# Kernel tuning notes

Hardware: AMD Instinct MI355X
Metric: run time of the kernel (lower is better)

The kernel has to match this reference:

```python
import jax, jax.numpy as jnp
import numpy as np

# Module hyperparameters (from init_kwargs / HGSELLayer defaults)
D_MODEL = 512
D_FF = 2048
N_EXPERTS = 64
K_ACTIVE = 2
N_HASHES = 4
LAYER_ID = 0
SALT = 0.0
BUCKET_SCALE = 8.0        # hash bucket width for projection-based hashing
CAPACITY_FACTOR = 1.25    # per-expert capacity slack (hash routing is near-uniform)


def setup_inputs() -> dict:
    key = jax.random.key(0)
    k0, k1, k2, k3 = jax.random.split(key, 4)
    B, S = 4, 2048
    hidden_states = jax.random.normal(k0, (B, S, D_MODEL), dtype=jnp.float32)
    # Fixed (non-learned) hash projection vectors of the MultiHashRouter
    W_hash = jax.random.normal(k1, (N_HASHES, D_MODEL), dtype=jnp.float32) / np.float32(np.sqrt(D_MODEL))
    # Expert bank parameters: per-expert MLP d_model -> d_ff -> d_model
    W1 = jax.random.normal(k2, (N_EXPERTS, D_MODEL, D_FF), dtype=jnp.float32) * np.float32(1.0 / np.sqrt(D_MODEL))
    b1 = jnp.zeros((N_EXPERTS, D_FF), dtype=jnp.float32)
    W2 = jax.random.normal(k3, (N_EXPERTS, D_FF, D_MODEL), dtype=jnp.float32) * np.float32(1.0 / np.sqrt(D_FF))
    b2 = jnp.zeros((N_EXPERTS, D_MODEL), dtype=jnp.float32)
    return {"hidden_states": hidden_states, "W_hash": W_hash, "W1": W1, "b1": b1, "W2": W2, "b2": b2}


def reference(hidden_states, W_hash, W1, b1, W2, b2):
    B, S, D = hidden_states.shape
    T = B * S
    x = hidden_states.reshape(T, D)

    # ---- MultiHashRouter: hash-based top-k expert selection (non-learned routing) ----
    scores = x @ W_hash.T                                   # [T, n_hashes]
    buckets = jnp.mod(
        jnp.floor(scores * BUCKET_SCALE + SALT).astype(jnp.int32) + LAYER_ID,
        N_EXPERTS,
    )                                                       # [T, n_hashes]
    selected = buckets[:, :K_ACTIVE]                        # [T, k]
    flat_e = selected.reshape(-1)                           # [T*k]

    # ---- Dispatch: capacity-bucketed gather into per-expert buffers ----
    C = int(np.ceil(T * K_ACTIVE / N_EXPERTS * CAPACITY_FACTOR))
    oh = jax.nn.one_hot(flat_e, N_EXPERTS, dtype=jnp.int32)          # [T*k, E]
    pos = jnp.sum((jnp.cumsum(oh, axis=0) - 1) * oh, axis=1)         # slot within expert
    valid = pos < C                                                   # [T*k]
    pos_c = jnp.clip(pos, 0, C - 1)
    x_rep = jnp.repeat(x, K_ACTIVE, axis=0)                           # [T*k, D]
    buf = jnp.zeros((N_EXPERTS, C, D), dtype=x.dtype).at[flat_e, pos_c].add(
        jnp.where(valid[:, None], x_rep, 0.0)
    )                                                                 # [E, C, D]

    # ---- ExpertBank: grouped per-expert MLP (gelu) ----
    h = jax.nn.gelu(jnp.einsum('ecd,edf->ecf', buf, W1) + b1[:, None, :], approximate=False)
    y = jnp.einsum('ecf,efd->ecd', h, W2) + b2[:, None, :]            # [E, C, D]

    # ---- Combine: gather back per token-expert pair, uniform mean over k ----
    out_pairs = jnp.where(valid[:, None], y[flat_e, pos_c], 0.0)      # [T*k, D]
    out = out_pairs.reshape(T, K_ACTIVE, D).mean(axis=1)              # [T, D]
    return out.reshape(B, S, D)
```

## Files before the change

### kernel.cpp

```cpp
#include <hip/hip_runtime.h>
#include <hip/hip_bf16.h>

#define T_TOK 8192
#define NSLOT 16384
#define DM 512
#define DF 2048
#define NEXP 64
#define CAP 320
#define MP 384

typedef __bf16 bf16_t;
typedef __bf16 bf16x8 __attribute__((ext_vector_type(8)));
typedef float floatx4 __attribute__((ext_vector_type(4)));

__global__ __launch_bounds__(256) void k_scores(const float* __restrict__ x,
        const float* __restrict__ Wh, int* __restrict__ e_arr, int* __restrict__ inv)
{
    int tid = threadIdx.x;
    if (tid < 10) inv[blockIdx.x * 10 + tid] = -1;
    int wid = tid >> 6, lane = tid & 63;
    int t = blockIdx.x * 4 + wid;
    const float4* xp = (const float4*)(x + (size_t)t * DM);
    float4 x0 = xp[lane * 2], x1 = xp[lane * 2 + 1];
    const float4* w0p = (const float4*)(Wh);
    const float4* w1p = (const float4*)(Wh + DM);
    float4 a0 = w0p[lane * 2], a1 = w0p[lane * 2 + 1];
    float4 b0 = w1p[lane * 2], b1 = w1p[lane * 2 + 1];
    float s0 = x0.x*a0.x + x0.y*a0.y + x0.z*a0.z + x0.w*a0.w
             + x1.x*a1.x + x1.y*a1.y + x1.z*a1.z + x1.w*a1.w;
    float s1 = x0.x*b0.x + x0.y*b0.y + x0.z*b0.z + x0.w*b0.w
             + x1.x*b1.x + x1.y*b1.y + x1.z*b1.z + x1.w*b1.w;
    #pragma unroll
    for (int off = 32; off; off >>= 1) {
        s0 += __shfl_xor(s0, off);
        s1 += __shfl_xor(s1, off);
    }
    if (lane == 0) {
        int q0 = ((int)floorf(s0 * 8.0f)) & 63;
        int q1 = ((int)floorf(s1 * 8.0f)) & 63;
        e_arr[2 * t]     = q0;
        e_arr[2 * t + 1] = q1;
    }
}

__global__ __launch_bounds__(256) void k_hist(const int* __restrict__ e_arr,
        int* __restrict__ rank_arr, int* __restrict__ hist_g)
{
    __shared__ int se[256];
    __shared__ int hist[64];
    int tid = threadIdx.x;
    if (tid < 64) hist[tid] = 0;
    __syncthreads();
    int s = blockIdx.x * 256 + tid;
    int e = e_arr[s];
    se[tid] = e;
    atomicAdd(&hist[e], 1);
    __syncthreads();
    int cnt = 0;
    for (int j = 0; j < 255; ++j)
        if (j < tid && se[j] == e) cnt++;
    rank_arr[s] = cnt;
    if (tid < 64) hist_g[blockIdx.x * 64 + tid] = hist[tid];
}

__global__ __launch_bounds__(256) void k_pos(const int* __restrict__ e_arr,
        const int* __restrict__ rank_arr, const int* __restrict__ hist_g,
        int* __restrict__ pos_arr, int* __restrict__ inv)
{
    __shared__ int base[64];
    int tid = threadIdx.x, c = blockIdx.x;
    if (tid < 64) {
        int run = 0;
        for (int cc = 0; cc < c; ++cc) run += hist_g[cc * 64 + tid];
        base[tid] = run;
    }
    __syncthreads();
    int s = c * 256 + tid;
    int e = e_arr[s];
    int p = base[e] + rank_arr[s];
    pos_arr[s] = p;
    if (p < CAP) inv[e * CAP + p] = s;
}

__global__ __launch_bounds__(256) void k_buf(const float* __restrict__ x,
        const int* __restrict__ inv, bf16_t* __restrict__ buf)
{
    int tid = threadIdx.x;
    int r = blockIdx.x * 4 + (tid >> 6);
    int lane = tid & 63;
    int e = r / MP, row = r % MP;
    int s = (row < CAP) ? inv[e * CAP + row] : -1;
    union { uint4 u; bf16_t h[8]; } pk;
    if (s >= 0) {
        int t = s >> 1;
        const float* xr = x + (size_t)t * DM + lane * 8;
        float4 f0 = *(const float4*)xr;
        float4 f1 = *(const float4*)(xr + 4);
        pk.h[0] = (bf16_t)f0.x; pk.h[1] = (bf16_t)f0.y;
        pk.h[2] = (bf16_t)f0.z; pk.h[3] = (bf16_t)f0.w;
        pk.h[4] = (bf16_t)f1.x; pk.h[5] = (bf16_t)f1.y;
        pk.h[6] = (bf16_t)f1.z; pk.h[7] = (bf16_t)f1.w;
    } else {
        pk.u.x = 0; pk.u.y = 0; pk.u.z = 0; pk.u.w = 0;
    }
    *(uint4*)(buf + (size_t)r * DM + lane * 8) = pk.u;
}

template<int M_TOT, int OSTR, int N_DIM, int K_DIM, bool GELU, bool OUT_BF16>
__global__ __launch_bounds__(256) void gemm_fused(const bf16_t* __restrict__ A,
        const float* __restrict__ B, const float* __restrict__ bias,
        void* __restrict__ OutP)
{
    constexpr int MT = (M_TOT + 127) / 128;
    constexpr int NT = N_DIM / 128;
    int bx = blockIdx.x;
    int e  = bx / (MT * NT);
    int rem = bx % (MT * NT);
    int mt = rem / NT;
    int nt = rem % NT;

    const bf16_t* Ae = A + (size_t)e * MP * K_DIM + (size_t)mt * 128 * K_DIM;
    const float*  Be = B + (size_t)e * K_DIM * N_DIM + nt * 128;
    const float*  be = bias + (size_t)e * N_DIM + nt * 128;

    __shared__ __align__(16) bf16_t As[128 * 64];
    __shared__ __align__(16) bf16_t Bs[128 * 64];

    int tid = threadIdx.x;
    int lane = tid & 63;
    int wid = tid >> 6;
    int qm = lane & 15;
    int quad = lane >> 4;
    int wm = (wid >> 1) * 64;
    int wn = (wid & 1) * 64;

    int srow = lane >> 3;
    int gl = (lane & 7) ^ srow;
    const bf16_t* aPtr = Ae + (size_t)(wid * 32 + srow) * K_DIM + gl * 8;

    int bkg = tid & 7;
    int bn  = (tid >> 3) * 4;
    const float* bPtr = Be + (size_t)(bkg * 8) * N_DIM + bn;

    uint4  aR[4];
    float4 bR[8];
    #pragma unroll
    for (int c = 0; c < 4; ++c)
        aR[c] = *(const uint4*)(aPtr + (size_t)c * 8 * K_DIM);
    #pragma unroll
    for (int p = 0; p < 8; ++p)
        bR[p] = *(const float4*)(bPtr + (size_t)p * N_DIM);

    floatx4 acc[4][4];
    #pragma unroll
    for (int i = 0; i < 4; ++i)
        #pragma unroll
        for (int j = 0; j < 4; ++j) acc[i][j] = (floatx4)0.0f;

    #pragma unroll 2
    for (int kk = 0; kk < K_DIM; kk += 64) {
        __syncthreads();
        #pragma unroll
        for (int c = 0; c < 4; ++c)
            *(uint4*)(As + ((wid * 4 + c) * 64 + lane) * 8) = aR[c];
        #pragma unroll
        for (int i = 0; i < 4; ++i) {
            union { uint4 u; bf16_t h[8]; } pk;
            #pragma unroll
            for (int p = 0; p < 8; ++p)
                pk.h[p] = (bf16_t)(((const float*)&bR[p])[i]);
            int r = bn + i;
            *(uint4*)(Bs + ((r * 8 + (bkg ^ (r & 7))) * 8)) = pk.u;
        }
        if (kk + 64 < K_DIM) {
            #pragma unroll
            for (int c = 0; c < 4; ++c)
                aR[c] = *(const uint4*)(aPtr + (size_t)c * 8 * K_DIM + (kk + 64));
            #pragma unroll
            for (int p = 0; p < 8; ++p)
                bR[p] = *(const float4*)(bPtr + (size_t)(kk + 64 + p) * N_DIM);
        }
        __syncthreads();
        #pragma unroll
        for (int ks = 0; ks < 2; ++ks) {
            bf16x8 af[4], bfr[4];
            #pragma unroll
            for (int i = 0; i < 4; ++i) {
                int r = wm + i * 16 + qm;
                int pg = r * 8 + ((ks * 4 + quad) ^ (r & 7));
                af[i] = *(const bf16x8*)(As + pg * 8);
            }
            #pragma unroll
            for (int j = 0; j < 4; ++j) {
                int r = wn + j * 16 + qm;
                int pg = r * 8 + ((ks * 4 + quad) ^ (r & 7));
                bfr[j] = *(const bf16x8*)(Bs + pg * 8);
            }
            #pragma unroll
            for (int i = 0; i < 4; ++i)
                #pragma unroll
                for (int j = 0; j < 4; ++j)
                    acc[i][j] = __builtin_amdgcn_mfma_f32_16x16x32_bf16(
                        bfr[j], af[i], acc[i][j], 0, 0, 0);
        }
    }

    #pragma unroll
    for (int i = 0; i < 4; ++i) {
        int gm = mt * 128 + wm + i * 16 + qm;
        if (gm < M_TOT) {
            #pragma unroll
            for (int j = 0; j < 4; ++j) {
                int ln0 = wn + j * 16 + quad * 4;
                float4 bz = *(const float4*)(be + ln0);
                float v[4];
                #pragma unroll
                for (int r = 0; r < 4; ++r) {
                    float t = acc[i][j][r] + ((const float*)&bz)[r];
                    if (GELU) t = 0.5f * t * (1.0f + erff(t * 0.70710678118654752f));
                    v[r] = t;
                }
                size_t idx = ((size_t)e * OSTR + gm) * N_DIM + nt * 128 + ln0;
                if (OUT_BF16) {
                    union { uint2 u; bf16_t h[4]; } pk;
                    pk.h[0] = (bf16_t)v[0]; pk.h[1] = (bf16_t)v[1];
                    pk.h[2] = (bf16_t)v[2]; pk.h[3] = (bf16_t)v[3];
                    *(uint2*)((bf16_t*)OutP + idx) = pk.u;
                } else {
                    float4 o; o.x = v[0]; o.y = v[1]; o.z = v[2]; o.w = v[3];
                    *(float4*)((float*)OutP + idx) = o;
                }
            }
        }
    }
}

__global__ __launch_bounds__(256) void k_gather(const float* __restrict__ y,
        const int* __restrict__ e_arr, const int* __restrict__ pos_arr,
        float* __restrict__ out)
{
    int tid = threadIdx.x;
    int t = blockIdx.x * 4 + (tid >> 6);
    int lane = tid & 63;
    float a[8];
    #pragma unroll
    for (int i = 0; i < 8; ++i) a[i] = 0.0f;
    #pragma unroll
    for (int k = 0; k < 2; ++k) {
        int s = 2 * t + k;
        int e = e_arr[s], p = pos_arr[s];
        if (p < CAP) {
            const float* yr = y + ((size_t)e * CAP + p) * DM + lane * 8;
            float4 f0 = *(const float4*)yr;
            float4 f1 = *(const float4*)(yr + 4);
            a[0] += f0.x; a[1] += f0.y; a[2] += f0.z; a[3] += f0.w;
            a[4] += f1.x; a[5] += f1.y; a[6] += f1.z; a[7] += f1.w;
        }
    }
    float4 o0, o1;
    o0.x = a[0] * 0.5f; o0.y = a[1] * 0.5f; o0.z = a[2] * 0.5f; o0.w = a[3] * 0.5f;
    o1.x = a[4] * 0.5f; o1.y = a[5] * 0.5f; o1.z = a[6] * 0.5f; o1.w = a[7] * 0.5f;
    float* orow = out + (size_t)t * DM + lane * 8;
    *(float4*)orow = o0;
    *(float4*)(orow + 4) = o1;
}

extern "C" void kernel_launch(void* const* d_in, const int* in_sizes, int n_in,
                              void* d_out, int out_size, void* d_ws, size_t ws_size,
                              hipStream_t stream)
{
    const float* x  = (const float*)d_in[0];
    const float* Wh = (const float*)d_in[1];
    const float* W1 = (const float*)d_in[2];
    const float* b1 = (const float*)d_in[3];
    const float* W2 = (const float*)d_in[4];
    const float* b2 = (const float*)d_in[5];
    float* out = (float*)d_out;

    char* p = (char*)d_ws;
    int*    e_arr  = (int*)p;    p += (size_t)NSLOT * 4;
    int*    rank_a = (int*)p;    p += (size_t)NSLOT * 4;
    int*    hist_g = (int*)p;    p += (size_t)64 * 64 * 4;
    int*    pos_a  = (int*)p;    p += (size_t)NSLOT * 4;
    int*    inv    = (int*)p;    p += (size_t)NEXP * CAP * 4;
    bf16_t* buf    = (bf16_t*)p;
    float*  ybuf   = (float*)p;  p += (size_t)NEXP * CAP * DM * 4;
    bf16_t* hbuf   = (bf16_t*)p; p += (size_t)NEXP * MP * DF * 2;

    k_scores<<<2048, 256, 0, stream>>>(x, Wh, e_arr, inv);
    k_hist<<<64, 256, 0, stream>>>(e_arr, rank_a, hist_g);
    k_pos<<<64, 256, 0, stream>>>(e_arr, rank_a, hist_g, pos_a, inv);
    k_buf<<<NEXP * MP / 4, 256, 0, stream>>>(x, inv, buf);

    gemm_fused<CAP, MP, DF, DM, true, true>
        <<<NEXP * 3 * (DF / 128), 256, 0, stream>>>(buf, W1, b1, (void*)hbuf);

    gemm_fused<CAP, CAP, DM, DF, false, false>
        <<<NEXP * 3 * (DM / 128), 256, 0, stream>>>(hbuf, W2, b2, (void*)ybuf);

    k_gather<<<2048, 256, 0, stream>>>(ybuf, e_arr, pos_a, out);
}
```

Measured before the change: 902.7 us.

## Double-buffer LDS in expert GEMMs, reorder grid, emit bf16 expert outputs

Rewrites the grouped expert GEMM with double-buffered shared memory and two register stages, so global loads run three tiles ahead and only one barrier is needed per K-tile. The block index now iterates experts in the inner dimension and M tiles in the outer one, which changes scheduling and weight reuse across blocks. The second GEMM writes bf16 instead of fp32 and leaves the b2 bias to the gather kernel, cutting the output write and gather read traffic in half. This adds LDS use and register pressure (launch bounds 256,2) and lowers the precision of the expert outputs.

```diff
diff --git a/kernel.cpp b/kernel.cpp
--- a/kernel.cpp
+++ b/kernel.cpp
@@ -12,6 +12,12 @@
 typedef __bf16 bf16_t;
 typedef __bf16 bf16x8 __attribute__((ext_vector_type(8)));
 typedef float floatx4 __attribute__((ext_vector_type(4)));
+
+__device__ __forceinline__ void lgkm0_barrier() {
+    asm volatile("s_waitcnt lgkmcnt(0)" ::: "memory");
+    __builtin_amdgcn_s_barrier();
+    asm volatile("" ::: "memory");
+}
 
 __global__ __launch_bounds__(256) void k_scores(const float* __restrict__ x,
         const float* __restrict__ Wh, int* __restrict__ e_arr, int* __restrict__ inv)
@@ -106,25 +112,24 @@
     *(uint4*)(buf + (size_t)r * DM + lane * 8) = pk.u;
 }
 
-template<int M_TOT, int OSTR, int N_DIM, int K_DIM, bool GELU, bool OUT_BF16>
-__global__ __launch_bounds__(256) void gemm_fused(const bf16_t* __restrict__ A,
+template<int M_TOT, int OSTR, int N_DIM, int K_DIM, bool GELU, bool BIAS, bool OUT_BF16>
+__global__ __launch_bounds__(256, 2) void gemm_pipe(const bf16_t* __restrict__ A,
         const float* __restrict__ B, const float* __restrict__ bias,
         void* __restrict__ OutP)
 {
-    constexpr int MT = (M_TOT + 127) / 128;
     constexpr int NT = N_DIM / 128;
+    constexpr int NTILE = K_DIM / 64;
     int bx = blockIdx.x;
-    int e  = bx / (MT * NT);
-    int rem = bx % (MT * NT);
-    int mt = rem / NT;
-    int nt = rem % NT;
+    int mt = bx / (NEXP * NT);
+    int g  = bx % (NEXP * NT);
+    int e  = g / NT;
+    int nt = g % NT;
 
     const bf16_t* Ae = A + (size_t)e * MP * K_DIM + (size_t)mt * 128 * K_DIM;
     const float*  Be = B + (size_t)e * K_DIM * N_DIM + nt * 128;
-    const float*  be = bias + (size_t)e * N_DIM + nt * 128;
-
-    __shared__ __align__(16) bf16_t As[128 * 64];
-    __shared__ __align__(16) bf16_t Bs[128 * 64];
+
+    __shared__ __align__(16) bf16_t As[2][128 * 64];
+    __shared__ __align__(16) bf16_t Bs[2][128 * 64];
 
     int tid = threadIdx.x;
     int lane = tid & 63;
@@ -137,19 +142,32 @@
     int srow = lane >> 3;
     int gl = (lane & 7) ^ srow;
     const bf16_t* aPtr = Ae + (size_t)(wid * 32 + srow) * K_DIM + gl * 8;
-
     int bkg = tid & 7;
     int bn  = (tid >> 3) * 4;
     const float* bPtr = Be + (size_t)(bkg * 8) * N_DIM + bn;
 
-    uint4  aR[4];
-    float4 bR[8];
-    #pragma unroll
-    for (int c = 0; c < 4; ++c)
-        aR[c] = *(const uint4*)(aPtr + (size_t)c * 8 * K_DIM);
-    #pragma unroll
-    for (int p = 0; p < 8; ++p)
-        bR[p] = *(const float4*)(bPtr + (size_t)p * N_DIM);
+    uint4  aS[2][4];
+    float4 bS[2][8];
+
+    #define LOAD_A(st, t_) { _Pragma("unroll") \
+        for (int c = 0; c < 4; ++c) \
+            aS[st][c] = *(const uint4*)(aPtr + (size_t)c * 8 * K_DIM + (t_) * 64); }
+    #define LOAD_B(st, t_) { _Pragma("unroll") \
+        for (int p = 0; p < 8; ++p) \
+            bS[st][p] = *(const float4*)(bPtr + (size_t)((t_) * 64 + p) * N_DIM); }
+    #define STAGE(lb, st) { \
+        _Pragma("unroll") \
+        for (int c = 0; c < 4; ++c) \
+            *(uint4*)(&As[lb][((wid * 4 + c) * 64 + lane) * 8]) = aS[st][c]; \
+        _Pragma("unroll") \
+        for (int i = 0; i < 4; ++i) { \
+            union { uint4 u; bf16_t h[8]; } pk; \
+            _Pragma("unroll") \
+            for (int p = 0; p < 8; ++p) \
+                pk.h[p] = (bf16_t)(((const float*)&bS[st][p])[i]); \
+            int r_ = bn + i; \
+            *(uint4*)(&Bs[lb][(r_ * 8 + (bkg ^ (r_ & 7))) * 8]) = pk.u; \
+        } }
 
     floatx4 acc[4][4];
     #pragma unroll
@@ -157,30 +175,19 @@
         #pragma unroll
         for (int j = 0; j < 4; ++j) acc[i][j] = (floatx4)0.0f;
 
-    #pragma unroll 2
-    for (int kk = 0; kk < K_DIM; kk += 64) {
-        __syncthreads();
-        #pragma unroll
-        for (int c = 0; c < 4; ++c)
-            *(uint4*)(As + ((wid * 4 + c) * 64 + lane) * 8) = aR[c];
-        #pragma unroll
-        for (int i = 0; i < 4; ++i) {
-            union { uint4 u; bf16_t h[8]; } pk;
-            #pragma unroll
-            for (int p = 0; p < 8; ++p)
-                pk.h[p] = (bf16_t)(((const float*)&bR[p])[i]);
-            int r = bn + i;
-            *(uint4*)(Bs + ((r * 8 + (bkg ^ (r & 7))) * 8)) = pk.u;
+    LOAD_A(0, 0); LOAD_B(0, 0);
+    STAGE(0, 0);
+    if (NTILE > 1) { LOAD_A(1, 1); LOAD_B(1, 1); }
+    if (NTILE > 2) { LOAD_A(0, 2); LOAD_B(0, 2); }
+    lgkm0_barrier();
+
+    for (int t = 0; t < NTILE; ++t) {
+        int cur = t & 1;
+        if (t + 1 < NTILE) {
+            int s = (t + 1) & 1;
+            STAGE(cur ^ 1, s);
+            if (t + 3 < NTILE) { LOAD_A(s, t + 3); LOAD_B(s, t + 3); }
         }
-        if (kk + 64 < K_DIM) {
-            #pragma unroll
-            for (int c = 0; c < 4; ++c)
-                aR[c] = *(const uint4*)(aPtr + (size_t)c * 8 * K_DIM + (kk + 64));
-            #pragma unroll
-            for (int p = 0; p < 8; ++p)
-                bR[p] = *(const float4*)(bPtr + (size_t)(kk + 64 + p) * N_DIM);
-        }
-        __syncthreads();
         #pragma unroll
         for (int ks = 0; ks < 2; ++ks) {
             bf16x8 af[4], bfr[4];
@@ -188,13 +195,13 @@
             for (int i = 0; i < 4; ++i) {
                 int r = wm + i * 16 + qm;
                 int pg = r * 8 + ((ks * 4 + quad) ^ (r & 7));
-                af[i] = *(const bf16x8*)(As + pg * 8);
+                af[i] = *(const bf16x8*)(&As[cur][pg * 8]);
             }
             #pragma unroll
             for (int j = 0; j < 4; ++j) {
                 int r = wn + j * 16 + qm;
                 int pg = r * 8 + ((ks * 4 + quad) ^ (r & 7));
-                bfr[j] = *(const bf16x8*)(Bs + pg * 8);
+                bfr[j] = *(const bf16x8*)(&Bs[cur][pg * 8]);
             }
             #pragma unroll
             for (int i = 0; i < 4; ++i)
@@ -203,7 +210,11 @@
                     acc[i][j] = __builtin_amdgcn_mfma_f32_16x16x32_bf16(
                         bfr[j], af[i], acc[i][j], 0, 0, 0);
         }
-    }
+        lgkm0_barrier();
+    }
+    #undef LOAD_A
+    #undef LOAD_B
+    #undef STAGE
 
     #pragma unroll
     for (int i = 0; i < 4; ++i) {
@@ -212,13 +223,18 @@
             #pragma unroll
             for (int j = 0; j < 4; ++j) {
                 int ln0 = wn + j * 16 + quad * 4;
-                float4 bz = *(const float4*)(be + ln0);
                 float v[4];
                 #pragma unroll
-                for (int r = 0; r < 4; ++r) {
-                    float t = acc[i][j][r] + ((const float*)&bz)[r];
-                    if (GELU) t = 0.5f * t * (1.0f + erff(t * 0.70710678118654752f));
-                    v[r] = t;
+                for (int r = 0; r < 4; ++r) v[r] = acc[i][j][r];
+                if (BIAS) {
+                    float4 bz = *(const float4*)(bias + (size_t)e * N_DIM + nt * 128 + ln0);
+                    #pragma unroll
+                    for (int r = 0; r < 4; ++r) v[r] += ((const float*)&bz)[r];
+                }
+                if (GELU) {
+                    #pragma unroll
+                    for (int r = 0; r < 4; ++r)
+                        v[r] = 0.5f * v[r] * (1.0f + erff(v[r] * 0.70710678118654752f));
                 }
                 size_t idx = ((size_t)e * OSTR + gm) * N_DIM + nt * 128 + ln0;
                 if (OUT_BF16) {
@@ -235,9 +251,9 @@
     }
 }
 
-__global__ __launch_bounds__(256) void k_gather(const float* __restrict__ y,
-        const int* __restrict__ e_arr, const int* __restrict__ pos_arr,
-        float* __restrict__ out)
+__global__ __launch_bounds__(256) void k_gather(const bf16_t* __restrict__ y,
+        const float* __restrict__ b2, const int* __restrict__ e_arr,
+        const int* __restrict__ pos_arr, float* __restrict__ out)
 {
     int tid = threadIdx.x;
     int t = blockIdx.x * 4 + (tid >> 6);
@@ -250,11 +266,15 @@
         int s = 2 * t + k;
         int e = e_arr[s], p = pos_arr[s];
         if (p < CAP) {
-            const float* yr = y + ((size_t)e * CAP + p) * DM + lane * 8;
-            float4 f0 = *(const float4*)yr;
-            float4 f1 = *(const float4*)(yr + 4);
-            a[0] += f0.x; a[1] += f0.y; a[2] += f0.z; a[3] += f0.w;
-            a[4] += f1.x; a[5] += f1.y; a[6] += f1.z; a[7] += f1.w;
+            union { uint4 u; bf16_t h[8]; } raw;
+            raw.u = *(const uint4*)(y + ((size_t)e * CAP + p) * DM + lane * 8);
+            const float* bz = b2 + (size_t)e * DM + lane * 8;
+            float4 z0 = ((const float4*)bz)[0];
+            float4 z1 = ((const float4*)bz)[1];
+            a[0] += (float)raw.h[0] + z0.x; a[1] += (float)raw.h[1] + z0.y;
+            a[2] += (float)raw.h[2] + z0.z; a[3] += (float)raw.h[3] + z0.w;
+            a[4] += (float)raw.h[4] + z1.x; a[5] += (float)raw.h[5] + z1.y;
+            a[6] += (float)raw.h[6] + z1.z; a[7] += (float)raw.h[7] + z1.w;
         }
     }
     float4 o0, o1;
@@ -284,7 +304,7 @@
     int*    pos_a  = (int*)p;    p += (size_t)NSLOT * 4;
     int*    inv    = (int*)p;    p += (size_t)NEXP * CAP * 4;
     bf16_t* buf    = (bf16_t*)p;
-    float*  ybuf   = (float*)p;  p += (size_t)NEXP * CAP * DM * 4;
+    bf16_t* ybuf   = (bf16_t*)p; p += (size_t)NEXP * MP * DM * 2;
     bf16_t* hbuf   = (bf16_t*)p; p += (size_t)NEXP * MP * DF * 2;
 
     k_scores<<<2048, 256, 0, stream>>>(x, Wh, e_arr, inv);
@@ -292,11 +312,11 @@
     k_pos<<<64, 256, 0, stream>>>(e_arr, rank_a, hist_g, pos_a, inv);
     k_buf<<<NEXP * MP / 4, 256, 0, stream>>>(x, inv, buf);
 
-    gemm_fused<CAP, MP, DF, DM, true, true>
+    gemm_pipe<CAP, MP, DF, DM, true, true, true>
         <<<NEXP * 3 * (DF / 128), 256, 0, stream>>>(buf, W1, b1, (void*)hbuf);
 
-    gemm_fused<CAP, CAP, DM, DF, false, false>
-        <<<NEXP * 3 * (DM / 128), 256, 0, stream>>>(hbuf, W2, b2, (void*)ybuf);
-
-    k_gather<<<2048, 256, 0, stream>>>(ybuf, e_arr, pos_a, out);
-}
+    gemm_pipe<CAP, CAP, DM, DF, false, false, true>
+        <<<NEXP * 3 * (DM / 128), 256, 0, stream>>>(hbuf, W2, nullptr, (void*)ybuf);
+
+    k_gather<<<2048, 256, 0, stream>>>(ybuf, b2, e_arr, pos_a, out);
+}
```

Measured after the change: 1.257 ms. +39.2%, slower.
